# Kernel tuning notes

Hardware: AMD Instinct MI355X
Metric: run time of the kernel (lower is better)

Reference implementation:

```python
import jax, jax.numpy as jnp
import numpy as np

B = 512          # batch
SIZE_IN = 1024   # input features
SIZE_OUT = 256   # output features
NUM_Q = 16       # quantiles


def setup_inputs() -> dict:
    key = jax.random.key(0)
    k1, k2, k3, k4 = jax.random.split(key, 4)
    x = jax.random.normal(k1, (B, SIZE_IN), dtype=jnp.float32)
    indices = jax.random.randint(k2, (B, SIZE_IN), 0, NUM_Q, dtype=jnp.int64)
    # param_index table: row (q*SIZE_IN + j) holds a SIZE_OUT weight vector
    param_table = jax.random.normal(k3, (NUM_Q * SIZE_IN, SIZE_OUT), dtype=jnp.float32)
    bias = jax.random.normal(k4, (SIZE_OUT,), dtype=jnp.float32)
    return {"x": x, "indices": indices, "param_table": param_table, "bias": bias}


def reference(x, indices, param_table, bias):
    size_in = x.shape[1]
    # flat row index into the quantile-indexed table: q*size_in + feature_pos
    flat_idx = indices * size_in + jnp.arange(size_in, dtype=indices.dtype)[None, :]  # [B, In]
    gathered = param_table[flat_idx]  # [B, In, Out] gather
    # scale each gathered weight vector by the scalar input and reduce over features
    out = jnp.einsum('bi,bio->bo', x, gathered)  # [B, Out]
    return out + bias
```

## Files before the change

### kernel.cpp

```cpp
#include <hip/hip_runtime.h>
#include <stdint.h>


constexpr int SIZE_IN  = 1024;
constexpr int SIZE_OUT = 256;
constexpr int BATCH    = 512;
constexpr int NUM_Q    = 16;
constexpr int TM = 32;
constexpr int TN = 128;
constexpr int A_STRIDE = 1032;

constexpr size_t WS_NEED = (size_t)NUM_Q * BATCH * SIZE_OUT * sizeof(float);

typedef short short8   __attribute__((ext_vector_type(8)));
typedef float floatx4  __attribute__((ext_vector_type(4)));

__device__ inline uint32_t pack2bf(float lo, float hi) {
    uint32_t a = __float_as_uint(lo) + 0x8000u;
    uint32_t b = __float_as_uint(hi) + 0x8000u;
    return __builtin_amdgcn_perm(b, a, 0x07060302);
}

template <bool USE_WS>
__global__ __launch_bounds__(256, 2)
void idxlin_mfma(const float* __restrict__ x,
                 const int*   __restrict__ idx,
                 const float* __restrict__ table,
                 const float* __restrict__ bias,
                 float*       __restrict__ out,
                 float*       __restrict__ ws)
{
    __shared__ uint16_t Alds[TM * A_STRIDE];

    const int tid = threadIdx.x;
    const int q   = blockIdx.x & 15;
    const int r   = blockIdx.x >> 4;
    const int nh  = r & 1;
    const int bt  = r >> 1;
    const int b0  = bt * TM;
    const int n0  = nh * TN;

    const float4* x4 = reinterpret_cast<const float4*>(x   + b0 * SIZE_IN);
    const int4*   i4 = reinterpret_cast<const int4*>(idx + b0 * SIZE_IN);
    #pragma unroll 4
    for (int s = 0; s < TM; ++s) {
        const int f = s * 256 + tid;
        const float4 xv = x4[f];
        const int4   iv = i4[f];
        const float v0 = (iv.x == q) ? xv.x : 0.f;
        const float v1 = (iv.y == q) ? xv.y : 0.f;
        const float v2 = (iv.z == q) ? xv.z : 0.f;
        const float v3 = (iv.w == q) ? xv.w : 0.f;
        uint2 d;
        d.x = pack2bf(v0, v1);
        d.y = pack2bf(v2, v3);
        *reinterpret_cast<uint2*>(&Alds[s * A_STRIDE + tid * 4]) = d;
    }
    __syncthreads();

    const int lane  = tid & 63;
    const int w     = tid >> 6;
    const int nlane = lane & 15;
    const int quad  = lane >> 4;

    const float* bp = table + (q * SIZE_IN + quad * 8) * SIZE_OUT + n0 + w * 32 + nlane;
    const uint16_t* arow0 = &Alds[(0 * 16 + nlane) * A_STRIDE + quad * 8];
    const uint16_t* arow1 = &Alds[(1 * 16 + nlane) * A_STRIDE + quad * 8];

    floatx4 acc[2][2] = {{{0.f,0.f,0.f,0.f},{0.f,0.f,0.f,0.f}},
                         {{0.f,0.f,0.f,0.f},{0.f,0.f,0.f,0.f}}};

    #pragma unroll 2
    for (int kb = 0; kb < SIZE_IN / 32; ++kb) {
        float wv[2][8];
        #pragma unroll
        for (int nt = 0; nt < 2; ++nt)
            #pragma unroll
            for (int j = 0; j < 8; ++j)
                wv[nt][j] = bp[j * SIZE_OUT + nt * 16];

        const short8 a0 = *reinterpret_cast<const short8*>(arow0 + kb * 32);
        const short8 a1 = *reinterpret_cast<const short8*>(arow1 + kb * 32);

        #pragma unroll
        for (int nt = 0; nt < 2; ++nt) {
            union { uint32_t u[4]; short8 s; } bf;
            bf.u[0] = pack2bf(wv[nt][0], wv[nt][1]);
            bf.u[1] = pack2bf(wv[nt][2], wv[nt][3]);
            bf.u[2] = pack2bf(wv[nt][4], wv[nt][5]);
            bf.u[3] = pack2bf(wv[nt][6], wv[nt][7]);
            acc[0][nt] = __builtin_amdgcn_mfma_f32_16x16x32_bf16(a0, bf.s, acc[0][nt], 0, 0, 0);
            acc[1][nt] = __builtin_amdgcn_mfma_f32_16x16x32_bf16(a1, bf.s, acc[1][nt], 0, 0, 0);
        }
        bp += 32 * SIZE_OUT;
    }

    if (USE_WS) {
        float* wsq = ws + ((size_t)(q * BATCH + b0)) * SIZE_OUT + n0;
        #pragma unroll
        for (int mt = 0; mt < 2; ++mt)
            #pragma unroll
            for (int nt = 0; nt < 2; ++nt)
                #pragma unroll
                for (int rr = 0; rr < 4; ++rr) {
                    const int row = mt * 16 + quad * 4 + rr;
                    const int col = w * 32 + nt * 16 + nlane;
                    wsq[row * SIZE_OUT + col] = acc[mt][nt][rr];
                }
    } else {
        #pragma unroll
        for (int mt = 0; mt < 2; ++mt)
            #pragma unroll
            for (int nt = 0; nt < 2; ++nt)
                #pragma unroll
                for (int rr = 0; rr < 4; ++rr) {
                    const int bg = b0 + mt * 16 + quad * 4 + rr;
                    const int o  = n0 + w * 32 + nt * 16 + nlane;
                    atomicAdd(&out[bg * SIZE_OUT + o], acc[mt][nt][rr]);
                }
        if (q == 0) {
            const int o_l = tid & (TN - 1);
            const int m0  = (tid >> 7) * 16;
            const float bv = bias[n0 + o_l];
            #pragma unroll
            for (int rr = 0; rr < 16; ++rr)
                atomicAdd(&out[(b0 + m0 + rr) * SIZE_OUT + n0 + o_l], bv);
        }
    }
}

__global__ __launch_bounds__(256)
void reduce_ws(const float* __restrict__ ws, const float* __restrict__ bias,
               float* __restrict__ out)
{
    const int e  = blockIdx.x * 256 + threadIdx.x;
    const int o4 = e & 63;
    const float4* w4 = reinterpret_cast<const float4*>(ws);
    float4 s = reinterpret_cast<const float4*>(bias)[o4];
    #pragma unroll
    for (int q = 0; q < NUM_Q; ++q) {
        const float4 v = w4[(size_t)q * (BATCH * SIZE_OUT / 4) + e];
        s.x += v.x; s.y += v.y; s.z += v.z; s.w += v.w;
    }
    reinterpret_cast<float4*>(out)[e] = s;
}

extern "C" void kernel_launch(void* const* d_in, const int* in_sizes, int n_in,
                              void* d_out, int out_size, void* d_ws, size_t ws_size,
                              hipStream_t stream) {
    const float* x     = (const float*)d_in[0];
    const int*   idx   = (const int*)d_in[1];
    const float* table = (const float*)d_in[2];
    const float* bias  = (const float*)d_in[3];
    float*       out   = (float*)d_out;
    float*       ws    = (float*)d_ws;

    if (ws_size >= WS_NEED) {
        idxlin_mfma<true><<<dim3(512), dim3(256), 0, stream>>>(x, idx, table, bias, out, ws);
        reduce_ws<<<dim3(BATCH * SIZE_OUT / 4 / 256), dim3(256), 0, stream>>>(ws, bias, out);
    } else {
        hipMemsetAsync(out, 0, (size_t)out_size * sizeof(float), stream);
        idxlin_mfma<false><<<dim3(512), dim3(256), 0, stream>>>(x, idx, table, bias, out, ws);
    }
}
```

Measured before the change: 89.83 us.

## Fuse quantile loop into single kernel and drop workspace reduction

Each block now iterates over all 16 quantiles, rebuilding the masked bf16 A tile per quantile and accumulating in registers, then writes output plus bias directly. This removes the large per-quantile workspace, the separate reduction kernel and the atomic fallback. The column tile is halved, and the grid shrinks from 512 to 64 blocks, greatly reducing parallelism and serialising the quantile loop within each block.

```diff
diff --git a/kernel.cpp b/kernel.cpp
--- a/kernel.cpp
+++ b/kernel.cpp
@@ -7,10 +7,8 @@
 constexpr int BATCH    = 512;
 constexpr int NUM_Q    = 16;
 constexpr int TM = 32;
-constexpr int TN = 128;
+constexpr int TN = 64;
 constexpr int A_STRIDE = 1032;
-
-constexpr size_t WS_NEED = (size_t)NUM_Q * BATCH * SIZE_OUT * sizeof(float);
 
 typedef short short8   __attribute__((ext_vector_type(8)));
 typedef float floatx4  __attribute__((ext_vector_type(4)));
@@ -21,128 +19,84 @@
     return __builtin_amdgcn_perm(b, a, 0x07060302);
 }
 
-template <bool USE_WS>
 __global__ __launch_bounds__(256, 2)
-void idxlin_mfma(const float* __restrict__ x,
-                 const int*   __restrict__ idx,
-                 const float* __restrict__ table,
-                 const float* __restrict__ bias,
-                 float*       __restrict__ out,
-                 float*       __restrict__ ws)
+void idxlin_fused(const float* __restrict__ x,
+                  const int*   __restrict__ idx,
+                  const float* __restrict__ table,
+                  const float* __restrict__ bias,
+                  float*       __restrict__ out)
 {
     __shared__ uint16_t Alds[TM * A_STRIDE];
 
     const int tid = threadIdx.x;
-    const int q   = blockIdx.x & 15;
-    const int r   = blockIdx.x >> 4;
-    const int nh  = r & 1;
-    const int bt  = r >> 1;
+    const int nh  = blockIdx.x & 3;
+    const int bt  = blockIdx.x >> 2;
     const int b0  = bt * TM;
     const int n0  = nh * TN;
-
-    const float4* x4 = reinterpret_cast<const float4*>(x   + b0 * SIZE_IN);
-    const int4*   i4 = reinterpret_cast<const int4*>(idx + b0 * SIZE_IN);
-    #pragma unroll 4
-    for (int s = 0; s < TM; ++s) {
-        const int f = s * 256 + tid;
-        const float4 xv = x4[f];
-        const int4   iv = i4[f];
-        const float v0 = (iv.x == q) ? xv.x : 0.f;
-        const float v1 = (iv.y == q) ? xv.y : 0.f;
-        const float v2 = (iv.z == q) ? xv.z : 0.f;
-        const float v3 = (iv.w == q) ? xv.w : 0.f;
-        uint2 d;
-        d.x = pack2bf(v0, v1);
-        d.y = pack2bf(v2, v3);
-        *reinterpret_cast<uint2*>(&Alds[s * A_STRIDE + tid * 4]) = d;
-    }
-    __syncthreads();
 
     const int lane  = tid & 63;
     const int w     = tid >> 6;
     const int nlane = lane & 15;
     const int quad  = lane >> 4;
 
-    const float* bp = table + (q * SIZE_IN + quad * 8) * SIZE_OUT + n0 + w * 32 + nlane;
+    const float4* x4 = reinterpret_cast<const float4*>(x   + b0 * SIZE_IN);
+    const int4*   i4 = reinterpret_cast<const int4*>(idx + b0 * SIZE_IN);
+
     const uint16_t* arow0 = &Alds[(0 * 16 + nlane) * A_STRIDE + quad * 8];
     const uint16_t* arow1 = &Alds[(1 * 16 + nlane) * A_STRIDE + quad * 8];
 
-    floatx4 acc[2][2] = {{{0.f,0.f,0.f,0.f},{0.f,0.f,0.f,0.f}},
-                         {{0.f,0.f,0.f,0.f},{0.f,0.f,0.f,0.f}}};
+    floatx4 acc[2] = {{0.f,0.f,0.f,0.f},{0.f,0.f,0.f,0.f}};
 
-    #pragma unroll 2
-    for (int kb = 0; kb < SIZE_IN / 32; ++kb) {
-        float wv[2][8];
-        #pragma unroll
-        for (int nt = 0; nt < 2; ++nt)
+    for (int q = 0; q < NUM_Q; ++q) {
+        __syncthreads();
+        #pragma unroll 4
+        for (int s = 0; s < TM; ++s) {
+            const int f = s * 256 + tid;
+            const float4 xv = x4[f];
+            const int4   iv = i4[f];
+            const float v0 = (iv.x == q) ? xv.x : 0.f;
+            const float v1 = (iv.y == q) ? xv.y : 0.f;
+            const float v2 = (iv.z == q) ? xv.z : 0.f;
+            const float v3 = (iv.w == q) ? xv.w : 0.f;
+            uint2 d;
+            d.x = pack2bf(v0, v1);
+            d.y = pack2bf(v2, v3);
+            *reinterpret_cast<uint2*>(&Alds[s * A_STRIDE + tid * 4]) = d;
+        }
+        __syncthreads();
+
+        const float* bp = table + (q * SIZE_IN + quad * 8) * SIZE_OUT
+                        + n0 + w * 16 + nlane;
+        #pragma unroll 2
+        for (int kb = 0; kb < SIZE_IN / 32; ++kb) {
+            float wv[8];
             #pragma unroll
             for (int j = 0; j < 8; ++j)
-                wv[nt][j] = bp[j * SIZE_OUT + nt * 16];
+                wv[j] = bp[j * SIZE_OUT];
 
-        const short8 a0 = *reinterpret_cast<const short8*>(arow0 + kb * 32);
-        const short8 a1 = *reinterpret_cast<const short8*>(arow1 + kb * 32);
+            const short8 a0 = *reinterpret_cast<const short8*>(arow0 + kb * 32);
+            const short8 a1 = *reinterpret_cast<const short8*>(arow1 + kb * 32);
 
-        #pragma unroll
-        for (int nt = 0; nt < 2; ++nt) {
             union { uint32_t u[4]; short8 s; } bf;
-            bf.u[0] = pack2bf(wv[nt][0], wv[nt][1]);
-            bf.u[1] = pack2bf(wv[nt][2], wv[nt][3]);
-            bf.u[2] = pack2bf(wv[nt][4], wv[nt][5]);
-            bf.u[3] = pack2bf(wv[nt][6], wv[nt][7]);
-            acc[0][nt] = __builtin_amdgcn_mfma_f32_16x16x32_bf16(a0, bf.s, acc[0][nt], 0, 0, 0);
-            acc[1][nt] = __builtin_amdgcn_mfma_f32_16x16x32_bf16(a1, bf.s, acc[1][nt], 0, 0, 0);
+            bf.u[0] = pack2bf(wv[0], wv[1]);
+            bf.u[1] = pack2bf(wv[2], wv[3]);
+            bf.u[2] = pack2bf(wv[4], wv[5]);
+            bf.u[3] = pack2bf(wv[6], wv[7]);
+            acc[0] = __builtin_amdgcn_mfma_f32_16x16x32_bf16(a0, bf.s, acc[0], 0, 0, 0);
+            acc[1] = __builtin_amdgcn_mfma_f32_16x16x32_bf16(a1, bf.s, acc[1], 0, 0, 0);
+            bp += 32 * SIZE_OUT;
         }
-        bp += 32 * SIZE_OUT;
     }
 
-    if (USE_WS) {
-        float* wsq = ws + ((size_t)(q * BATCH + b0)) * SIZE_OUT + n0;
+    const int col = n0 + w * 16 + nlane;
+    const float bv = bias[col];
+    #pragma unroll
+    for (int mt = 0; mt < 2; ++mt)
         #pragma unroll
-        for (int mt = 0; mt < 2; ++mt)
-            #pragma unroll
-            for (int nt = 0; nt < 2; ++nt)
-                #pragma unroll
-                for (int rr = 0; rr < 4; ++rr) {
-                    const int row = mt * 16 + quad * 4 + rr;
-                    const int col = w * 32 + nt * 16 + nlane;
-                    wsq[row * SIZE_OUT + col] = acc[mt][nt][rr];
-                }
-    } else {
-        #pragma unroll
-        for (int mt = 0; mt < 2; ++mt)
-            #pragma unroll
-            for (int nt = 0; nt < 2; ++nt)
-                #pragma unroll
-                for (int rr = 0; rr < 4; ++rr) {
-                    const int bg = b0 + mt * 16 + quad * 4 + rr;
-                    const int o  = n0 + w * 32 + nt * 16 + nlane;
-                    atomicAdd(&out[bg * SIZE_OUT + o], acc[mt][nt][rr]);
-                }
-        if (q == 0) {
-            const int o_l = tid & (TN - 1);
-            const int m0  = (tid >> 7) * 16;
-            const float bv = bias[n0 + o_l];
-            #pragma unroll
-            for (int rr = 0; rr < 16; ++rr)
-                atomicAdd(&out[(b0 + m0 + rr) * SIZE_OUT + n0 + o_l], bv);
+        for (int rr = 0; rr < 4; ++rr) {
+            const int row = b0 + mt * 16 + quad * 4 + rr;
+            out[row * SIZE_OUT + col] = acc[mt][rr] + bv;
         }
-    }
-}
-
-__global__ __launch_bounds__(256)
-void reduce_ws(const float* __restrict__ ws, const float* __restrict__ bias,
-               float* __restrict__ out)
-{
-    const int e  = blockIdx.x * 256 + threadIdx.x;
-    const int o4 = e & 63;
-    const float4* w4 = reinterpret_cast<const float4*>(ws);
-    float4 s = reinterpret_cast<const float4*>(bias)[o4];
-    #pragma unroll
-    for (int q = 0; q < NUM_Q; ++q) {
-        const float4 v = w4[(size_t)q * (BATCH * SIZE_OUT / 4) + e];
-        s.x += v.x; s.y += v.y; s.z += v.z; s.w += v.w;
-    }
-    reinterpret_cast<float4*>(out)[e] = s;
 }
 
 extern "C" void kernel_launch(void* const* d_in, const int* in_sizes, int n_in,
@@ -153,13 +107,8 @@
     const float* table = (const float*)d_in[2];
     const float* bias  = (const float*)d_in[3];
     float*       out   = (float*)d_out;
-    float*       ws    = (float*)d_ws;
+    (void)d_ws; (void)ws_size;
 
-    if (ws_size >= WS_NEED) {
-        idxlin_mfma<true><<<dim3(512), dim3(256), 0, stream>>>(x, idx, table, bias, out, ws);
-        reduce_ws<<<dim3(BATCH * SIZE_OUT / 4 / 256), dim3(256), 0, stream>>>(ws, bias, out);
-    } else {
-        hipMemsetAsync(out, 0, (size_t)out_size * sizeof(float), stream);
-        idxlin_mfma<false><<<dim3(512), dim3(256), 0, stream>>>(x, idx, table, bias, out, ws);
-    }
+    idxlin_fused<<<dim3((BATCH / TM) * (SIZE_OUT / TN)), dim3(256), 0, stream>>>(
+        x, idx, table, bias, out);
 }
```

After: 218.6 us. 2.43x slower.
